# Performance work log

Measured on AMD Instinct MI355X. Metric: run time of the kernel, lower is better.

Reference implementation:

```python
import jax, jax.numpy as jnp
import numpy as np

VOCAB = 100000
D = 128
B = 256
L = 2048  # leaves per tree (power of two -> complete binary tree)


def setup_inputs() -> dict:
    key = jax.random.key(0)
    k1, k2, k3, k4 = jax.random.split(key, 4)
    word_ids = jax.random.randint(k1, (B, L), 0, VOCAB)
    embedding = jax.random.normal(k2, (VOCAB, D), dtype=jnp.float32) * 0.1
    # torch nn.Linear(2*D, D): weight [D, 2*D], bias [D]
    W = jax.random.normal(k3, (D, 2 * D), dtype=jnp.float32) * (1.0 / np.sqrt(2 * D))
    b = jax.random.normal(k4, (D,), dtype=jnp.float32) * 0.01
    return {"word_ids": word_ids, "embedding": embedding, "W": W, "b": b}


def reference(word_ids, embedding, W, b):
    # Leaves: embedding lookup for every leaf of every tree. [B, L, D]
    x = embedding[word_ids]
    # Internal nodes, batched by depth: each level combines adjacent pairs
    # via linear(concat(left, right)). log2(L) levels (static unroll).
    while x.shape[1] > 1:
        left = x[:, 0::2, :]   # [B, n/2, D]
        right = x[:, 1::2, :]  # [B, n/2, D]
        pair = jnp.concatenate([left, right], axis=-1)  # [B, n/2, 2D]
        x = jnp.einsum('bnd,od->bno', pair, W) + b      # [B, n/2, D]
    return x[:, 0, :]  # root result per tree, [B, D]
```

## Files before the change

kernel.cpp:

```cpp
#include <hip/hip_runtime.h>


typedef __bf16 bf16x8 __attribute__((ext_vector_type(8)));
typedef __bf16 bf16x4 __attribute__((ext_vector_type(4)));
typedef float f32x4 __attribute__((ext_vector_type(4)));

#define STRIDE 136

#define BARRIER() do {                                          \
    asm volatile("s_waitcnt lgkmcnt(0)" ::: "memory");          \
    __builtin_amdgcn_s_barrier();                               \
} while (0)

__global__ void prep_kernel(const float* __restrict__ W,
                            const float* __restrict__ bias,
                            const float* __restrict__ emb,
                            __bf16* __restrict__ wpack1,
                            __bf16* __restrict__ wpack2,
                            float* __restrict__ b2,
                            __bf16* __restrict__ etab, int n8) {
    const int tid = threadIdx.x;
    const int bx = blockIdx.x;
    const int wv = tid >> 6, l = tid & 63;
    if (bx < 16) {
        const int nl = bx >> 3, kk = bx & 7;
        const int o = ((wv << 1) + nl) * 16 + (l & 15);
        const int d = kk * 32 + ((l >> 4) << 3);
        const float* src = W + o * 256 + d;
        bf16x8 h;
#pragma unroll
        for (int j = 0; j < 8; ++j) h[j] = (__bf16)src[j];
        *(bf16x8*)(wpack1 + (size_t)(bx * 256 + tid) * 8) = h;
    } else if (bx < 48) {
        const int f2 = bx - 16;
        const int nl = f2 >> 4, kk = f2 & 15;
        const int o = ((wv << 1) + nl) * 16 + (l & 15);
        const int d = kk * 32 + ((l >> 4) << 3);
        const int s = d >> 7, c = d & 127;
        const float* wrow = W + o * 256 + (s >> 1) * 128;
        const float* wcol = W + (s & 1) * 128 + c;
        float a8[8] = {0, 0, 0, 0, 0, 0, 0, 0};
        for (int k = 0; k < 128; ++k) {
            const float wl = wrow[k];
            const float* wr = wcol + k * 256;
#pragma unroll
            for (int j = 0; j < 8; ++j) a8[j] += wl * wr[j];
        }
        bf16x8 h;
#pragma unroll
        for (int j = 0; j < 8; ++j) h[j] = (__bf16)a8[j];
        *(bf16x8*)(wpack2 + (size_t)(f2 * 256 + tid) * 8) = h;
    } else if (bx == 48) {
        if (tid < 128) {
            float acc = bias[tid];
            const float* wr = W + tid * 256;
            for (int k = 0; k < 128; ++k)
                acc += (wr[k] + wr[128 + k]) * bias[k];
            b2[tid] = acc;
        }
    }
    const int stride = gridDim.x * blockDim.x;
    for (int i = bx * blockDim.x + tid; i < n8; i += stride) {
        const float* s = emb + (size_t)i * 8;
        const f32x4 a = *(const f32x4*)s;
        const f32x4 b = *(const f32x4*)(s + 4);
        const bf16x4 ha = __builtin_convertvector(a, bf16x4);
        const bf16x4 hb = __builtin_convertvector(b, bf16x4);
        bf16x8 h;
#pragma unroll
        for (int j = 0; j < 4; ++j) { h[j] = ha[j]; h[4 + j] = hb[j]; }
        *(bf16x8*)(etab + (size_t)i * 8) = h;
    }
}

template <int NOUT>
__device__ __forceinline__ void quad_acc_stream(
    const __bf16* src, const bf16x8* wres, const bf16x8* wp2,
    const float* b2v, int tid, int q, int lm, f32x4 (&acc)[2])
{
    const int me = (NOUT >= 16) ? lm : (lm < NOUT ? lm : 0);
    acc[0] = f32x4{ b2v[0], b2v[0], b2v[0], b2v[0] };
    acc[1] = f32x4{ b2v[1], b2v[1], b2v[1], b2v[1] };
#pragma unroll
    for (int kk = 0; kk < 16; ++kk) {
        const bf16x8 af = *(const bf16x8*)
            &src[((kk >> 2) * NOUT + me) * STRIDE + (kk & 3) * 32 + q * 8];
        acc[0] = __builtin_amdgcn_mfma_f32_16x16x32_bf16(
            af, wres[kk], acc[0], 0, 0, 0);
        acc[1] = __builtin_amdgcn_mfma_f32_16x16x32_bf16(
            af, wp2[(16 + kk) * 256 + tid], acc[1], 0, 0, 0);
    }
}

template <int NOUT>
__device__ __forceinline__ void quad_acc_res(
    const __bf16* src, const bf16x8* w2r,
    const float* b2v, int q, int lm, f32x4 (&acc)[2])
{
    const int me = (NOUT >= 16) ? lm : (lm < NOUT ? lm : 0);
    acc[0] = f32x4{ b2v[0], b2v[0], b2v[0], b2v[0] };
    acc[1] = f32x4{ b2v[1], b2v[1], b2v[1], b2v[1] };
#pragma unroll
    for (int kk = 0; kk < 16; ++kk) {
        const bf16x8 af = *(const bf16x8*)
            &src[((kk >> 2) * NOUT + me) * STRIDE + (kk & 3) * 32 + q * 8];
        acc[0] = __builtin_amdgcn_mfma_f32_16x16x32_bf16(
            af, w2r[kk], acc[0], 0, 0, 0);
        acc[1] = __builtin_amdgcn_mfma_f32_16x16x32_bf16(
            af, w2r[16 + kk], acc[1], 0, 0, 0);
    }
}

__device__ __forceinline__ void gissue_bf(
    const int (&ids)[4], const __bf16* etab, int tid, bf16x8 (&st)[4])
{
#pragma unroll
    for (int i = 0; i < 4; ++i)
        st[i] = *(const bf16x8*)(etab + (size_t)ids[i] * 128 + (tid & 15) * 8);
}
__device__ __forceinline__ void gwrite_bf(
    __bf16* dst, int tid, const bf16x8 (&st)[4])
{
#pragma unroll
    for (int i = 0; i < 4; ++i) {
        const int row = 16 * i + (tid >> 4);
        *(bf16x8*)&dst[row * STRIDE + (tid & 15) * 8] = st[i];
    }
}

__device__ __forceinline__ void gissue_f32(
    const int* wb64, const float* emb, int tid, f32x4 (&st)[8])
{
#pragma unroll
    for (int i = 0; i < 8; ++i) {
        const int rt = (tid >> 5) + 8 * i;
        const int id = wb64[4 * (rt & 15) + (rt >> 4)];
        st[i] = *(const f32x4*)(emb + (size_t)id * 128 + (tid & 31) * 4);
    }
}
__device__ __forceinline__ void gwrite_f32(
    __bf16* dst, int tid, const f32x4 (&st)[8])
{
#pragma unroll
    for (int i = 0; i < 8; ++i) {
        const int rt = (tid >> 5) + 8 * i;
        *(bf16x4*)&dst[rt * STRIDE + (tid & 31) * 4] =
            __builtin_convertvector(st[i], bf16x4);
    }
}

template <bool BF>
__global__ __launch_bounds__(256, 3) void tree128_kernel(
    const int* __restrict__ wid, const float* __restrict__ emb,
    const __bf16* __restrict__ etab, const __bf16* __restrict__ wpack2,
    const float* __restrict__ b2, __bf16* __restrict__ yout)
{
    __shared__ __align__(16) __bf16 bufA[64 * STRIDE];
    __shared__ __align__(16) __bf16 bufB[64 * STRIDE];
    __shared__ __align__(16) __bf16 bufD[64 * STRIDE];
    const int tid = threadIdx.x;
    const int batch = blockIdx.x >> 3;
    const int pair = blockIdx.x & 7;
    const int wv = tid >> 6, ln = tid & 63, q = ln >> 4, lm = ln & 15;

    const bf16x8* wp2 = (const bf16x8*)wpack2;
    bf16x8 wres[16];
#pragma unroll
    for (int f = 0; f < 16; ++f) wres[f] = wp2[f * 256 + tid];
    float b2v[2];
    b2v[0] = b2[(2 * wv + 0) * 16 + lm];
    b2v[1] = b2[(2 * wv + 1) * 16 + lm];

    const int* wb = wid + batch * 2048 + pair * 256;

    auto L12 = [&](const __bf16* src, int c) {
        f32x4 a2[2];
        quad_acc_stream<16>(src, wres, wp2, b2v, tid, q, lm, a2);
#pragma unroll
        for (int nl = 0; nl < 2; ++nl) {
            const int col = (2 * wv + nl) * 16 + lm;
            const bf16x4 hv = __builtin_convertvector(a2[nl], bf16x4);
#pragma unroll
            for (int r = 0; r < 4; ++r)
                bufD[(r * 16 + 4 * c + q) * STRIDE + col] = hv[r];
        }
    };

    if constexpr (BF) {
        int ids[4][4];
#pragma unroll
        for (int c = 0; c < 4; ++c)
#pragma unroll
            for (int i = 0; i < 4; ++i)
                ids[c][i] = wb[64 * c + 4 * (tid >> 4) + i];
        bf16x8 s1[4], s2[4];
        gissue_bf(ids[0], etab, tid, s1);
        gissue_bf(ids[1], etab, tid, s2);
        gwrite_bf(bufA, tid, s1);
        BARRIER();
        gissue_bf(ids[2], etab, tid, s1);
        L12(bufA, 0);
        gwrite_bf(bufB, tid, s2);
        BARRIER();
        gissue_bf(ids[3], etab, tid, s2);
        L12(bufB, 1);
        gwrite_bf(bufA, tid, s1);
        BARRIER();
        L12(bufA, 2);
        gwrite_bf(bufB, tid, s2);
        BARRIER();
        L12(bufB, 3);
        BARRIER();
    } else {
        f32x4 st[8];
        gissue_f32(wb, emb, tid, st);
        gwrite_f32(bufA, tid, st);
        BARRIER();
        gissue_f32(wb + 64, emb, tid, st);
        L12(bufA, 0);
        gwrite_f32(bufB, tid, st);
        BARRIER();
        gissue_f32(wb + 128, emb, tid, st);
        L12(bufB, 1);
        gwrite_f32(bufA, tid, st);
        BARRIER();
        gissue_f32(wb + 192, emb, tid, st);
        L12(bufA, 2);
        gwrite_f32(bufB, tid, st);
        BARRIER();
        L12(bufB, 3);
        BARRIER();
    }

    {
        f32x4 a2[2];
        quad_acc_stream<16>(bufD, wres, wp2, b2v, tid, q, lm, a2);
#pragma unroll
        for (int nl = 0; nl < 2; ++nl) {
            const int col = (2 * wv + nl) * 16 + lm;
            const bf16x4 hv = __builtin_convertvector(a2[nl], bf16x4);
#pragma unroll
            for (int r = 0; r < 4; ++r)
                bufA[(r * 4 + q) * STRIDE + col] = hv[r];
        }
    }
    BARRIER();
    {
        f32x4 a2[2];
        quad_acc_stream<4>(bufA, wres, wp2, b2v, tid, q, lm, a2);
        __bf16* yrow = yout + (size_t)(batch * 32 + pair * 4) * 128;
#pragma unroll
        for (int nl = 0; nl < 2; ++nl) {
            const int col = (2 * wv + nl) * 16 + lm;
            if (q == 0) {
#pragma unroll
                for (int r = 0; r < 4; ++r)
                    yrow[r * 128 + col] = (__bf16)a2[nl][r];
            }
        }
    }
}

__global__ __launch_bounds__(256) void tree32_kernel(
    const __bf16* __restrict__ yin, const __bf16* __restrict__ wpack1,
    const __bf16* __restrict__ wpack2, const float* __restrict__ b2,
    const float* __restrict__ bias, float* __restrict__ out)
{
    __shared__ __align__(16) __bf16 buf0[32 * STRIDE];
    __shared__ __align__(16) __bf16 buf1[8 * STRIDE];
    const int tid = threadIdx.x;
    const int batch = blockIdx.x;
    const int wv = tid >> 6, ln = tid & 63, q = ln >> 4, lm = ln & 15;

    bf16x8 w2r[32];
    const bf16x8* wp2 = (const bf16x8*)wpack2;
#pragma unroll
    for (int f = 0; f < 32; ++f) w2r[f] = wp2[f * 256 + tid];
    bf16x8 w1r[16];
    const bf16x8* wp1 = (const bf16x8*)wpack1;
#pragma unroll
    for (int f = 0; f < 16; ++f) w1r[f] = wp1[f * 256 + tid];
    float b2v[2], b1v[2];
    b2v[0] = b2[(2 * wv + 0) * 16 + lm];
    b2v[1] = b2[(2 * wv + 1) * 16 + lm];
    b1v[0] = bias[(2 * wv + 0) * 16 + lm];
    b1v[1] = bias[(2 * wv + 1) * 16 + lm];

#pragma unroll
    for (int i = 0; i < 2; ++i) {
        const int flat = tid + 256 * i;
        const int o = flat >> 4;
        const int c8 = flat & 15;
        const bf16x8 v =
            *(const bf16x8*)(yin + (size_t)(batch * 32 + o) * 128 + c8 * 8);
        *(bf16x8*)&buf0[((o & 3) * 8 + (o >> 2)) * STRIDE + c8 * 8] = v;
    }
    __syncthreads();

    {
        f32x4 a2[2];
        quad_acc_res<8>(buf0, w2r, b2v, q, lm, a2);
#pragma unroll
        for (int nl = 0; nl < 2; ++nl) {
            const int col = (2 * wv + nl) * 16 + lm;
            const bf16x4 hv = __builtin_convertvector(a2[nl], bf16x4);
            if (q < 2) {
#pragma unroll
                for (int r = 0; r < 4; ++r)
                    buf1[(r * 2 + q) * STRIDE + col] = hv[r];
            }
        }
    }
    __syncthreads();
    {
        f32x4 a2[2];
        quad_acc_res<2>(buf1, w2r, b2v, q, lm, a2);
#pragma unroll
        for (int nl = 0; nl < 2; ++nl) {
            const int col = (2 * wv + nl) * 16 + lm;
            const bf16x4 hv = __builtin_convertvector(a2[nl], bf16x4);
            if (q == 0) {
#pragma unroll
                for (int r = 0; r < 2; ++r)
                    buf0[r * STRIDE + col] = hv[r];
            }
        }
    }
    __syncthreads();
    {
        f32x4 acc[2];
        acc[0] = f32x4{ b1v[0], b1v[0], b1v[0], b1v[0] };
        acc[1] = f32x4{ b1v[1], b1v[1], b1v[1], b1v[1] };
#pragma unroll
        for (int kh = 0; kh < 2; ++kh) {
            bf16x8 af[4];
#pragma unroll
            for (int j = 0; j < 4; ++j)
                af[j] = *(const bf16x8*)&buf0[kh * STRIDE + j * 32 + q * 8];
#pragma unroll
            for (int nl = 0; nl < 2; ++nl)
#pragma unroll
                for (int j = 0; j < 4; ++j)
                    acc[nl] = __builtin_amdgcn_mfma_f32_16x16x32_bf16(
                        af[j], w1r[nl * 8 + kh * 4 + j], acc[nl], 0, 0, 0);
        }
#pragma unroll
        for (int nl = 0; nl < 2; ++nl) {
            const int col = (2 * wv + nl) * 16 + lm;
            if (q == 0) out[(size_t)batch * 128 + col] = acc[nl][0];
        }
    }
}

extern "C" void kernel_launch(void* const* d_in, const int* in_sizes, int n_in,
                              void* d_out, int out_size, void* d_ws, size_t ws_size,
                              hipStream_t stream) {
    const int*   wid = (const int*)d_in[0];
    const float* emb = (const float*)d_in[1];
    const float* W   = (const float*)d_in[2];
    const float* b   = (const float*)d_in[3];
    float* out = (float*)d_out;

    __bf16* wpack1 = (__bf16*)d_ws;
    __bf16* wpack2 = wpack1 + 32768;
    float*  b2     = (float*)(wpack2 + 65536);
    __bf16* y      = (__bf16*)(b2 + 128);
    __bf16* etab   = y + 256 * 32 * 128;

    const size_t need_full = (size_t)(32768 + 65536) * 2 + 512
                           + (size_t)256 * 32 * 128 * 2
                           + (size_t)100000 * 128 * 2;
    const bool bf = (ws_size >= need_full);
    const int n8 = bf ? (100000 * 128 / 8) : 0;

    prep_kernel<<<2048, 256, 0, stream>>>(W, b, emb, wpack1, wpack2, b2,
                                          etab, n8);
    if (bf)
        tree128_kernel<true><<<2048, 256, 0, stream>>>(
            wid, emb, etab, wpack2, b2, y);
    else
        tree128_kernel<false><<<2048, 256, 0, stream>>>(
            wid, emb, etab, wpack2, b2, y);
    tree32_kernel<<<256, 256, 0, stream>>>(y, wpack1, wpack2, b2, b, out);
}
```

Before: 158.3 us.

## Gather embeddings via direct global-to-LDS DMA with XOR-swizzled unpadded tiles

The leaf-level kernel now issues the bf16 embedding gathers as global_load_lds DMA transfers straight into shared memory. This replaces the register round-trip followed by LDS stores, and waits on vmcnt at the barriers. To suit the DMA's contiguous write pattern, the LDS tiles drop their padded stride for an XOR-swizzled 128-wide layout with a permuted leaf-to-row mapping. All 32 weight fragments are also kept in registers instead of streaming half from global memory. In exchange, register pressure rises under the 3-block launch bound, and the index remapping and swizzle must stay consistent across every level.

```diff
diff --git a/kernel.cpp b/kernel.cpp
--- a/kernel.cpp
+++ b/kernel.cpp
@@ -11,6 +11,17 @@
     asm volatile("s_waitcnt lgkmcnt(0)" ::: "memory");          \
     __builtin_amdgcn_s_barrier();                               \
 } while (0)
+
+#define VMBARRIER(N) do {                                                   \
+    asm volatile("s_waitcnt vmcnt(" #N ") lgkmcnt(0)" ::: "memory");        \
+    __builtin_amdgcn_s_barrier();                                           \
+} while (0)
+
+__device__ __forceinline__ void dma16(const __bf16* g, __bf16* l) {
+    __builtin_amdgcn_global_load_lds(
+        (const __attribute__((address_space(1))) unsigned int*)g,
+        (__attribute__((address_space(3))) unsigned int*)l, 16, 0, 0);
+}
 
 __global__ void prep_kernel(const float* __restrict__ W,
                             const float* __restrict__ bias,
@@ -74,21 +85,158 @@
 }
 
 template <int NOUT>
-__device__ __forceinline__ void quad_acc_stream(
-    const __bf16* src, const bf16x8* wres, const bf16x8* wp2,
-    const float* b2v, int tid, int q, int lm, f32x4 (&acc)[2])
+__device__ __forceinline__ void quad_acc_swz(
+    const __bf16* src, const bf16x8* w2r, const float* b2v,
+    int q, int lm, f32x4 (&a2)[2])
 {
     const int me = (NOUT >= 16) ? lm : (lm < NOUT ? lm : 0);
-    acc[0] = f32x4{ b2v[0], b2v[0], b2v[0], b2v[0] };
-    acc[1] = f32x4{ b2v[1], b2v[1], b2v[1], b2v[1] };
+    a2[0] = f32x4{ b2v[0], b2v[0], b2v[0], b2v[0] };
+    a2[1] = f32x4{ b2v[1], b2v[1], b2v[1], b2v[1] };
 #pragma unroll
     for (int kk = 0; kk < 16; ++kk) {
-        const bf16x8 af = *(const bf16x8*)
-            &src[((kk >> 2) * NOUT + me) * STRIDE + (kk & 3) * 32 + q * 8];
-        acc[0] = __builtin_amdgcn_mfma_f32_16x16x32_bf16(
-            af, wres[kk], acc[0], 0, 0, 0);
-        acc[1] = __builtin_amdgcn_mfma_f32_16x16x32_bf16(
-            af, wp2[(16 + kk) * 256 + tid], acc[1], 0, 0, 0);
+        const int s = kk >> 2;
+        const int row = 2 * me + (s & 1) + 32 * (s >> 1);
+        const int cph = ((kk & 3) * 4 + q) ^ (me & 7);
+        const bf16x8 af = *(const bf16x8*)&src[row * 128 + cph * 8];
+        a2[0] = __builtin_amdgcn_mfma_f32_16x16x32_bf16(
+            af, w2r[kk], a2[0], 0, 0, 0);
+        a2[1] = __builtin_amdgcn_mfma_f32_16x16x32_bf16(
+            af, w2r[16 + kk], a2[1], 0, 0, 0);
+    }
+}
+
+template <bool BF>
+__global__ __launch_bounds__(256, 3) void tree128_kernel(
+    const int* __restrict__ wid, const float* __restrict__ emb,
+    const __bf16* __restrict__ etab, const __bf16* __restrict__ wpack2,
+    const float* __restrict__ b2, __bf16* __restrict__ yout)
+{
+    __shared__ __align__(16) __bf16 bufA[64 * 128];
+    __shared__ __align__(16) __bf16 bufB[64 * 128];
+    __shared__ __align__(16) __bf16 bufD[64 * 128];
+    const int tid = threadIdx.x;
+    const int batch = blockIdx.x >> 3;
+    const int pair = blockIdx.x & 7;
+    const int wv = tid >> 6, ln = tid & 63, q = ln >> 4, lm = ln & 15;
+
+    const bf16x8* wp2 = (const bf16x8*)wpack2;
+    bf16x8 w2r[32];
+#pragma unroll
+    for (int f = 0; f < 32; ++f) w2r[f] = wp2[f * 256 + tid];
+    float b2v[2];
+    b2v[0] = b2[(2 * wv + 0) * 16 + lm];
+    b2v[1] = b2[(2 * wv + 1) * 16 + lm];
+
+    const int* wb = wid + batch * 2048 + pair * 256;
+
+    auto L12 = [&](const __bf16* src, int c) {
+        f32x4 a2[2];
+        quad_acc_swz<16>(src, w2r, b2v, q, lm, a2);
+        const int X = (4 * c + q) & 7;
+#pragma unroll
+        for (int nl = 0; nl < 2; ++nl) {
+            const int col = (2 * wv + nl) * 16 + lm;
+            const bf16x4 hv = __builtin_convertvector(a2[nl], bf16x4);
+#pragma unroll
+            for (int r = 0; r < 4; ++r) {
+                const int row = 8 * c + 2 * q + (r & 1) + 32 * (r >> 1);
+                bufD[row * 128 + (col ^ (X << 3))] = hv[r];
+            }
+        }
+    };
+
+    if constexpr (BF) {
+        int ids[4][4];
+        int rowk[4];
+#pragma unroll
+        for (int k = 0; k < 4; ++k) {
+            const int row = 16 * wv + 4 * k + (ln >> 4);
+            rowk[k] = row;
+            const int leaf = ((row & 31) >> 1) * 4 + (row >> 5) * 2 + (row & 1);
+#pragma unroll
+            for (int g = 0; g < 4; ++g) ids[g][k] = wb[g * 64 + leaf];
+        }
+        __builtin_amdgcn_sched_barrier(0);
+
+        auto ISSUE = [&](const int (&idk)[4], __bf16* buf) {
+#pragma unroll
+            for (int k = 0; k < 4; ++k) {
+                const int c16 = (ln & 15) ^ ((rowk[k] >> 1) & 7);
+                const __bf16* gp = etab + (size_t)idk[k] * 128 + c16 * 8;
+                __bf16* lp = buf + (16 * wv + 4 * k) * 128;
+                dma16(gp, lp);
+            }
+        };
+
+        ISSUE(ids[0], bufA);
+        ISSUE(ids[1], bufB);
+        VMBARRIER(4);
+        L12(bufA, 0);
+        VMBARRIER(0);
+        ISSUE(ids[2], bufA);
+        L12(bufB, 1);
+        VMBARRIER(0);
+        ISSUE(ids[3], bufB);
+        L12(bufA, 2);
+        VMBARRIER(0);
+        L12(bufB, 3);
+        BARRIER();
+    } else {
+        f32x4 st[8];
+        auto GISS = [&](int g) {
+#pragma unroll
+            for (int i = 0; i < 8; ++i) {
+                const int row = (tid >> 5) + 8 * i;
+                const int leaf =
+                    ((row & 31) >> 1) * 4 + (row >> 5) * 2 + (row & 1);
+                const int id = wb[g * 64 + leaf];
+                st[i] = *(const f32x4*)(emb + (size_t)id * 128 + (tid & 31) * 4);
+            }
+        };
+        auto GWR = [&](__bf16* dst) {
+#pragma unroll
+            for (int i = 0; i < 8; ++i) {
+                const int row = (tid >> 5) + 8 * i;
+                const int X = (row >> 1) & 7;
+                *(bf16x4*)&dst[row * 128 + (((tid & 31) * 4) ^ (X << 3))] =
+                    __builtin_convertvector(st[i], bf16x4);
+            }
+        };
+        GISS(0); GWR(bufA); BARRIER();
+        GISS(1); L12(bufA, 0); GWR(bufB); BARRIER();
+        GISS(2); L12(bufB, 1); GWR(bufA); BARRIER();
+        GISS(3); L12(bufA, 2); GWR(bufB); BARRIER();
+        L12(bufB, 3); BARRIER();
+    }
+
+    {
+        f32x4 a2[2];
+        quad_acc_swz<16>(bufD, w2r, b2v, q, lm, a2);
+#pragma unroll
+        for (int nl = 0; nl < 2; ++nl) {
+            const int col = (2 * wv + nl) * 16 + lm;
+            const bf16x4 hv = __builtin_convertvector(a2[nl], bf16x4);
+#pragma unroll
+            for (int r = 0; r < 4; ++r) {
+                const int row = 2 * q + (r & 1) + 32 * (r >> 1);
+                bufA[row * 128 + (col ^ (q << 3))] = hv[r];
+            }
+        }
+    }
+    BARRIER();
+    {
+        f32x4 a2[2];
+        quad_acc_swz<4>(bufA, w2r, b2v, q, lm, a2);
+        __bf16* yrow = yout + (size_t)(batch * 32 + pair * 4) * 128;
+#pragma unroll
+        for (int nl = 0; nl < 2; ++nl) {
+            const int col = (2 * wv + nl) * 16 + lm;
+            if (q == 0) {
+#pragma unroll
+                for (int r = 0; r < 4; ++r)
+                    yrow[r * 128 + col] = (__bf16)a2[nl][r];
+            }
+        }
     }
 }
 
@@ -108,156 +256,6 @@
             af, w2r[kk], acc[0], 0, 0, 0);
         acc[1] = __builtin_amdgcn_mfma_f32_16x16x32_bf16(
             af, w2r[16 + kk], acc[1], 0, 0, 0);
-    }
-}
-
-__device__ __forceinline__ void gissue_bf(
-    const int (&ids)[4], const __bf16* etab, int tid, bf16x8 (&st)[4])
-{
-#pragma unroll
-    for (int i = 0; i < 4; ++i)
-        st[i] = *(const bf16x8*)(etab + (size_t)ids[i] * 128 + (tid & 15) * 8);
-}
-__device__ __forceinline__ void gwrite_bf(
-    __bf16* dst, int tid, const bf16x8 (&st)[4])
-{
-#pragma unroll
-    for (int i = 0; i < 4; ++i) {
-        const int row = 16 * i + (tid >> 4);
-        *(bf16x8*)&dst[row * STRIDE + (tid & 15) * 8] = st[i];
-    }
-}
-
-__device__ __forceinline__ void gissue_f32(
-    const int* wb64, const float* emb, int tid, f32x4 (&st)[8])
-{
-#pragma unroll
-    for (int i = 0; i < 8; ++i) {
-        const int rt = (tid >> 5) + 8 * i;
-        const int id = wb64[4 * (rt & 15) + (rt >> 4)];
-        st[i] = *(const f32x4*)(emb + (size_t)id * 128 + (tid & 31) * 4);
-    }
-}
-__device__ __forceinline__ void gwrite_f32(
-    __bf16* dst, int tid, const f32x4 (&st)[8])
-{
-#pragma unroll
-    for (int i = 0; i < 8; ++i) {
-        const int rt = (tid >> 5) + 8 * i;
-        *(bf16x4*)&dst[rt * STRIDE + (tid & 31) * 4] =
-            __builtin_convertvector(st[i], bf16x4);
-    }
-}
-
-template <bool BF>
-__global__ __launch_bounds__(256, 3) void tree128_kernel(
-    const int* __restrict__ wid, const float* __restrict__ emb,
-    const __bf16* __restrict__ etab, const __bf16* __restrict__ wpack2,
-    const float* __restrict__ b2, __bf16* __restrict__ yout)
-{
-    __shared__ __align__(16) __bf16 bufA[64 * STRIDE];
-    __shared__ __align__(16) __bf16 bufB[64 * STRIDE];
-    __shared__ __align__(16) __bf16 bufD[64 * STRIDE];
-    const int tid = threadIdx.x;
-    const int batch = blockIdx.x >> 3;
-    const int pair = blockIdx.x & 7;
-    const int wv = tid >> 6, ln = tid & 63, q = ln >> 4, lm = ln & 15;
-
-    const bf16x8* wp2 = (const bf16x8*)wpack2;
-    bf16x8 wres[16];
-#pragma unroll
-    for (int f = 0; f < 16; ++f) wres[f] = wp2[f * 256 + tid];
-    float b2v[2];
-    b2v[0] = b2[(2 * wv + 0) * 16 + lm];
-    b2v[1] = b2[(2 * wv + 1) * 16 + lm];
-
-    const int* wb = wid + batch * 2048 + pair * 256;
-
-    auto L12 = [&](const __bf16* src, int c) {
-        f32x4 a2[2];
-        quad_acc_stream<16>(src, wres, wp2, b2v, tid, q, lm, a2);
-#pragma unroll
-        for (int nl = 0; nl < 2; ++nl) {
-            const int col = (2 * wv + nl) * 16 + lm;
-            const bf16x4 hv = __builtin_convertvector(a2[nl], bf16x4);
-#pragma unroll
-            for (int r = 0; r < 4; ++r)
-                bufD[(r * 16 + 4 * c + q) * STRIDE + col] = hv[r];
-        }
-    };
-
-    if constexpr (BF) {
-        int ids[4][4];
-#pragma unroll
-        for (int c = 0; c < 4; ++c)
-#pragma unroll
-            for (int i = 0; i < 4; ++i)
-                ids[c][i] = wb[64 * c + 4 * (tid >> 4) + i];
-        bf16x8 s1[4], s2[4];
-        gissue_bf(ids[0], etab, tid, s1);
-        gissue_bf(ids[1], etab, tid, s2);
-        gwrite_bf(bufA, tid, s1);
-        BARRIER();
-        gissue_bf(ids[2], etab, tid, s1);
-        L12(bufA, 0);
-        gwrite_bf(bufB, tid, s2);
-        BARRIER();
-        gissue_bf(ids[3], etab, tid, s2);
-        L12(bufB, 1);
-        gwrite_bf(bufA, tid, s1);
-        BARRIER();
-        L12(bufA, 2);
-        gwrite_bf(bufB, tid, s2);
-        BARRIER();
-        L12(bufB, 3);
-        BARRIER();
-    } else {
-        f32x4 st[8];
-        gissue_f32(wb, emb, tid, st);
-        gwrite_f32(bufA, tid, st);
-        BARRIER();
-        gissue_f32(wb + 64, emb, tid, st);
-        L12(bufA, 0);
-        gwrite_f32(bufB, tid, st);
-        BARRIER();
-        gissue_f32(wb + 128, emb, tid, st);
-        L12(bufB, 1);
-        gwrite_f32(bufA, tid, st);
-        BARRIER();
-        gissue_f32(wb + 192, emb, tid, st);
-        L12(bufA, 2);
-        gwrite_f32(bufB, tid, st);
-        BARRIER();
-        L12(bufB, 3);
-        BARRIER();
-    }
-
-    {
-        f32x4 a2[2];
-        quad_acc_stream<16>(bufD, wres, wp2, b2v, tid, q, lm, a2);
-#pragma unroll
-        for (int nl = 0; nl < 2; ++nl) {
-            const int col = (2 * wv + nl) * 16 + lm;
-            const bf16x4 hv = __builtin_convertvector(a2[nl], bf16x4);
-#pragma unroll
-            for (int r = 0; r < 4; ++r)
-                bufA[(r * 4 + q) * STRIDE + col] = hv[r];
-        }
-    }
-    BARRIER();
-    {
-        f32x4 a2[2];
-        quad_acc_stream<4>(bufA, wres, wp2, b2v, tid, q, lm, a2);
-        __bf16* yrow = yout + (size_t)(batch * 32 + pair * 4) * 128;
-#pragma unroll
-        for (int nl = 0; nl < 2; ++nl) {
-            const int col = (2 * wv + nl) * 16 + lm;
-            if (q == 0) {
-#pragma unroll
-                for (int r = 0; r < 4; ++r)
-                    yrow[r * 128 + col] = (__bf16)a2[nl][r];
-            }
-        }
     }
 }
 
```

Measured after the change: 191.3 us. +20.8%, slower.
